# Optimization experiments

Measured on AMD Instinct MI355X. Metric: run time of the kernel, lower is better.

## Reference

```python
import jax, jax.numpy as jnp
import numpy as np

B, T, H, NH, HD = 2, 2048, 2048, 16, 128


def setup_inputs() -> dict:
    key = jax.random.key(0)
    k1, k2, k3 = jax.random.split(key, 3)
    hidden_states = jax.random.normal(k1, (B, T, H), dtype=jnp.float32)
    w_qkv = jax.random.normal(k2, (3 * H, H), dtype=jnp.float32) * (1.0 / np.sqrt(H))
    w_out = jax.random.normal(k3, (H, H), dtype=jnp.float32) * (1.0 / np.sqrt(H))
    return {"hidden_states": hidden_states, "w_qkv": w_qkv, "w_out": w_out}


def reference(hidden_states, w_qkv, w_out):
    scale = 1.0 / np.sqrt(HD)
    # qkv projection: torch Linear is x @ W.T with W [out, in]
    qkv = jnp.einsum('bth,oh->bto', hidden_states, w_qkv)  # [B, T, 3H]
    q, k, v = jnp.split(qkv, 3, axis=2)
    # [B, NH, T, HD]
    q = q.reshape(B, T, NH, HD).transpose(0, 2, 1, 3)
    k = k.reshape(B, T, NH, HD).transpose(0, 2, 1, 3)
    v = v.reshape(B, T, NH, HD).transpose(0, 2, 1, 3)
    scores = jnp.einsum('bhqd,bhkd->bhqk', q, k) * scale  # [B, NH, T, T]
    mask = jnp.tril(jnp.ones((T, T), dtype=bool))  # causal
    scores = jnp.where(mask[None, None], scores, -jnp.inf)
    probs = jax.nn.softmax(scores, axis=-1)
    attn = jnp.einsum('bhqk,bhkd->bhqd', probs, v)  # [B, NH, T, HD]
    attn = attn.transpose(0, 2, 1, 3).reshape(B, T, H)
    out = jnp.einsum('bth,oh->bto', attn, w_out)
    return out
```

## Files before the change

### kernel.cpp

```cpp
#include <hip/hip_runtime.h>
#include <cstdint>
#include <cstddef>

typedef _Float16 f16x8 __attribute__((ext_vector_type(8)));
typedef _Float16 f16x4 __attribute__((ext_vector_type(4)));
typedef float    f32x4 __attribute__((ext_vector_type(4)));
typedef unsigned short ushort_t;

#define LOG2E 1.4426950408889634f

constexpr int BATCH = 2;
constexpr int TSEQ  = 2048;
constexpr int HID   = 2048;
constexpr int NH    = 16;
constexpr int HD    = 128;
constexpr int GK    = 2048;
constexpr int NKT   = GK / 64;

__device__ inline f32x4 mfma16(f16x8 a, f16x8 b, f32x4 c) {
    return __builtin_amdgcn_mfma_f32_16x16x32_f16(a, b, c, 0, 0, 0);
}

__device__ inline void async_copy16(const void* src, void* dst_lds) {
    __builtin_amdgcn_global_load_lds(
        (const __attribute__((address_space(1))) uint32_t*)src,
        (__attribute__((address_space(3))) uint32_t*)dst_lds, 16, 0, 0);
}

__global__ __launch_bounds__(256)
void cast_f32_f16(const float4* __restrict__ in, f16x4* __restrict__ out, int n4) {
    int i = blockIdx.x * 256 + threadIdx.x;
    if (i >= n4) return;
    float4 v = in[i];
    f16x4 o = { (_Float16)v.x, (_Float16)v.y, (_Float16)v.z, (_Float16)v.w };
    out[i] = o;
}

template <int MODE>
__global__ __launch_bounds__(512, 2)
void gemm_bt(const _Float16* __restrict__ A, const _Float16* __restrict__ B,
             float* __restrict__ C, _Float16* __restrict__ Qo,
             _Float16* __restrict__ Ko, _Float16* __restrict__ Vo, int NB) {
    __shared__ __align__(16) _Float16 As[3][256 * 64];
    __shared__ __align__(16) _Float16 Bs[3][128 * 64];

    const int tid  = threadIdx.x;
    const int lane = tid & 63;
    const int w    = tid >> 6;
    const int l15  = lane & 15;
    const int lq   = lane >> 4;
    const int wr   = w >> 1, wc = w & 1;

    const int bid = (int)blockIdx.x;
    const int cpx = (int)gridDim.x >> 3;
    const int swz = (bid & 7) * cpx + (bid >> 3);
    const int bn  = swz % NB, bm = swz / NB;
    const int m0  = bm * 256, n0 = bn * 128;

    const _Float16* Ab = A + (size_t)m0 * GK;
    const _Float16* Bb = B + (size_t)n0 * GK;

    auto stage = [&](int t, int b) {
        const int k0 = t * 64;
        #pragma unroll
        for (int it = 0; it < 4; ++it) {
            const int slot = it * 512 + tid;
            const int row = slot >> 3, c16 = slot & 7;
            const int srcb = c16 ^ (row & 7);
            async_copy16(Ab + (size_t)row * GK + k0 + srcb * 8,
                         (char*)As[b] + slot * 16);
        }
        #pragma unroll
        for (int it = 0; it < 2; ++it) {
            const int slot = it * 512 + tid;
            const int row = slot >> 3, c16 = slot & 7;
            const int srcb = c16 ^ (row & 7);
            async_copy16(Bb + (size_t)row * GK + k0 + srcb * 8,
                         (char*)Bs[b] + slot * 16);
        }
    };

    f32x4 acc[4][4] = {};

    stage(0, 0);
    stage(1, 1);

    for (int t = 0; t < NKT; ++t) {
        if (t + 1 < NKT) asm volatile("s_waitcnt vmcnt(6)" ::: "memory");
        else             asm volatile("s_waitcnt vmcnt(0)" ::: "memory");
        __builtin_amdgcn_s_barrier();
        __builtin_amdgcn_sched_barrier(0);

        const char* At_ = (const char*)As[t % 3];
        const char* Bt_ = (const char*)Bs[t % 3];

        f16x8 af[4][2], bff[4][2];
        #pragma unroll
        for (int i = 0; i < 4; ++i)
            #pragma unroll
            for (int kk = 0; kk < 2; ++kk) {
                const int ra = wr * 64 + i * 16 + l15;
                af[i][kk]  = *(const f16x8*)(At_ + ra * 128 + (((kk * 4 + lq) ^ (ra & 7)) << 4));
                const int rb = wc * 64 + i * 16 + l15;
                bff[i][kk] = *(const f16x8*)(Bt_ + rb * 128 + (((kk * 4 + lq) ^ (rb & 7)) << 4));
            }

        if (t + 2 < NKT) stage(t + 2, (t + 2) % 3);

        __builtin_amdgcn_s_setprio(1);
        #pragma unroll
        for (int kk = 0; kk < 2; ++kk)
            #pragma unroll
            for (int i = 0; i < 4; ++i)
                #pragma unroll
                for (int j = 0; j < 4; ++j)
                    acc[i][j] = mfma16(af[i][kk], bff[j][kk], acc[i][j]);
        __builtin_amdgcn_s_setprio(0);
    }

    if (MODE == 0) {
        #pragma unroll
        for (int j = 0; j < 4; ++j) {
            const int ncol = n0 + wc * 64 + j * 16 + l15;
            const int which = ncol >> 11;
            const int oo = ncol & 2047;
            const int head = oo >> 7;
            const int d = oo & 127;
            _Float16* dst = (which == 0) ? Qo : (which == 1) ? Ko : Vo;
            const float scl = (which == 0) ? 0.08838834764831845f : 1.0f;
            #pragma unroll
            for (int i = 0; i < 4; ++i) {
                #pragma unroll
                for (int r = 0; r < 4; ++r) {
                    const int m = m0 + wr * 64 + i * 16 + lq * 4 + r;
                    const int b = m >> 11, tt = m & 2047;
                    dst[((size_t)(b * NH + head) * TSEQ + tt) * HD + d] =
                        (_Float16)(acc[i][j][r] * scl);
                }
            }
        }
    } else {
        #pragma unroll
        for (int i = 0; i < 4; ++i)
            #pragma unroll
            for (int j = 0; j < 4; ++j)
                #pragma unroll
                for (int r = 0; r < 4; ++r) {
                    const int m = m0 + wr * 64 + i * 16 + lq * 4 + r;
                    const int n = n0 + wc * 64 + j * 16 + l15;
                    C[(size_t)m * HID + n] = acc[i][j][r];
                }
    }
}

__global__ __launch_bounds__(512)
void attn_fwd(const _Float16* __restrict__ Q, const _Float16* __restrict__ K,
              const _Float16* __restrict__ V, _Float16* __restrict__ O) {
    __shared__ __align__(16) char Ks[2][64 * 256];
    __shared__ __align__(16) char Vt[2][128 * 128];
    __shared__ __align__(16) char Ps[8][2048];

    const int tid  = threadIdx.x;
    const int lane = tid & 63;
    const int w    = tid >> 6;
    const int l15  = lane & 15;
    const int lq   = lane >> 4;

    const int bh   = (int)blockIdx.x & 31;
    const int pair = (int)blockIdx.x >> 5;
    const int b = bh >> 4, h = bh & 15;

    const size_t base = (size_t)bh * TSEQ * HD;
    const _Float16* Qp = Q + base;
    const _Float16* Kp = K + base;
    const _Float16* Vp = V + base;

    uint4 vv[2];
    auto loadV = [&](int t) {
        #pragma unroll
        for (int it = 0; it < 2; ++it) {
            const int c8 = it * 8 + w;
            vv[it] = *(const uint4*)(Vp + (size_t)(t * 64 + lane) * HD + c8 * 8);
        }
    };
    auto stageK = [&](int t, int buf) {
        #pragma unroll
        for (int it = 0; it < 2; ++it) {
            const int slot = it * 512 + tid;
            const int row = slot >> 4, c16 = slot & 15;
            const int srcb = c16 ^ (row & 7);
            async_copy16(Kp + (size_t)(t * 64 + row) * HD + srcb * 8, Ks[buf] + slot * 16);
        }
    };
    auto writeV = [&](int buf) {
        #pragma unroll
        for (int it = 0; it < 2; ++it) {
            const int c8 = it * 8 + w;
            const uint32_t wrd[4] = {vv[it].x, vv[it].y, vv[it].z, vv[it].w};
            #pragma unroll
            for (int p2 = 0; p2 < 4; ++p2) {
                const int d0 = c8 * 8 + p2 * 2, d1 = d0 + 1;
                int b0 = d0 * 128 + lane * 2; b0 ^= (d0 & 7) << 4;
                int b1 = d1 * 128 + lane * 2; b1 ^= (d1 & 7) << 4;
                *(ushort_t*)(Vt[buf] + b0) = (ushort_t)(wrd[p2] & 0xffffu);
                *(ushort_t*)(Vt[buf] + b1) = (ushort_t)(wrd[p2] >> 16);
            }
        }
    };

    char* Pb = Ps[w];

    for (int phase = 0; phase < 2; ++phase) {
        const int qt = phase ? pair : (15 - pair);
        const int q0 = qt * 128;
        const int NT = 2 * qt + 2;

        if (phase) __syncthreads();

        const int qrow = q0 + w * 16 + l15;
        f16x8 qf[4];
        #pragma unroll
        for (int ks = 0; ks < 4; ++ks)
            qf[ks] = *(const f16x8*)(Qp + (size_t)qrow * HD + ks * 32 + lq * 8);

        f32x4 o[8] = {};
        float m_run[4], l_run[4];
        #pragma unroll
        for (int r = 0; r < 4; ++r) { m_run[r] = -1e30f; l_run[r] = 0.0f; }

        loadV(0);
        stageK(0, 0);

        int cur = 0;
        for (int t = 0; t < NT; ++t) {
            writeV(cur);
            __syncthreads();
            if (t + 1 < NT) {
                loadV(t + 1);
                stageK(t + 1, cur ^ 1);
            }

            const int kv0 = t * 64;
            f32x4 s[4] = {};
            __builtin_amdgcn_s_setprio(1);
            #pragma unroll
            for (int ks = 0; ks < 4; ++ks) {
                #pragma unroll
                for (int nf = 0; nf < 4; ++nf) {
                    const int r   = nf * 16 + l15;
                    const int blk = (ks * 4 + lq) ^ (r & 7);
                    const f16x8 kf = *(const f16x8*)(Ks[cur] + r * 256 + blk * 16);
                    s[nf] = mfma16(qf[ks], kf, s[nf]);
                }
            }
            __builtin_amdgcn_s_setprio(0);

            if (kv0 + 63 > q0 + w * 16) {
                #pragma unroll
                for (int nf = 0; nf < 4; ++nf) {
                    const int kvp = kv0 + nf * 16 + l15;
                    #pragma unroll
                    for (int r = 0; r < 4; ++r)
                        if (kvp > q0 + w * 16 + lq * 4 + r) s[nf][r] = -1e30f;
                }
            }

            float tmax[4];
            bool need = false;
            #pragma unroll
            for (int r = 0; r < 4; ++r) {
                float v = fmaxf(fmaxf(s[0][r], s[1][r]), fmaxf(s[2][r], s[3][r]));
                v = fmaxf(v, __shfl_xor(v, 1));
                v = fmaxf(v, __shfl_xor(v, 2));
                v = fmaxf(v, __shfl_xor(v, 4));
                v = fmaxf(v, __shfl_xor(v, 8));
                tmax[r] = v;
                need = need || (v > m_run[r] + 5.0f);
            }
            if (__any(need)) {
                float alpha[4];
                #pragma unroll
                for (int r = 0; r < 4; ++r) {
                    const float mn = fmaxf(m_run[r], tmax[r]);
                    alpha[r] = __builtin_exp2f((m_run[r] - mn) * LOG2E);
                    m_run[r] = mn;
                    l_run[r] *= alpha[r];
                }
                #pragma unroll
                for (int df = 0; df < 8; ++df)
                    #pragma unroll
                    for (int r = 0; r < 4; ++r)
                        o[df][r] *= alpha[r];
            }

            float ps[4] = {0.f, 0.f, 0.f, 0.f};
            #pragma unroll
            for (int nf = 0; nf < 4; ++nf) {
                #pragma unroll
                for (int r = 0; r < 4; ++r) {
                    const float p = __builtin_exp2f((s[nf][r] - m_run[r]) * LOG2E);
                    ps[r] += p;
                    const int qp = lq * 4 + r;
                    int byt = qp * 128 + (nf * 16 + l15) * 2;
                    byt ^= (qp & 7) << 4;
                    union { _Float16 hf; ushort_t u; } cv;
                    cv.hf = (_Float16)p;
                    *(ushort_t*)(Pb + byt) = cv.u;
                }
            }
            #pragma unroll
            for (int r = 0; r < 4; ++r) {
                float v = ps[r];
                v += __shfl_xor(v, 1);
                v += __shfl_xor(v, 2);
                v += __shfl_xor(v, 4);
                v += __shfl_xor(v, 8);
                l_run[r] += v;
            }

            __builtin_amdgcn_s_setprio(1);
            #pragma unroll
            for (int ks2 = 0; ks2 < 2; ++ks2) {
                const int pblk = (ks2 * 4 + lq) ^ (l15 & 7);
                const f16x8 pf = *(const f16x8*)(Pb + l15 * 128 + pblk * 16);
                #pragma unroll
                for (int df = 0; df < 8; ++df) {
                    const int vr   = df * 16 + l15;
                    const int vblk = (ks2 * 4 + lq) ^ (vr & 7);
                    const f16x8 vf = *(const f16x8*)(Vt[cur] + vr * 128 + vblk * 16);
                    o[df] = mfma16(pf, vf, o[df]);
                }
            }
            __builtin_amdgcn_s_setprio(0);
            cur ^= 1;
        }

        #pragma unroll
        for (int r = 0; r < 4; ++r) l_run[r] = 1.0f / l_run[r];
        #pragma unroll
        for (int df = 0; df < 8; ++df) {
            #pragma unroll
            for (int r = 0; r < 4; ++r) {
                const int qg = q0 + w * 16 + lq * 4 + r;
                const int dg = df * 16 + l15;
                O[((size_t)(b * TSEQ + qg)) * HID + h * HD + dg] =
                    (_Float16)(o[df][r] * l_run[r]);
            }
        }
    }
}

extern "C" void kernel_launch(void* const* d_in, const int* in_sizes, int n_in,
                              void* d_out, int out_size, void* d_ws, size_t ws_size,
                              hipStream_t stream) {
    (void)in_sizes; (void)n_in; (void)out_size; (void)ws_size;
    const float* hs   = (const float*)d_in[0];
    const float* wqkv = (const float*)d_in[1];
    const float* wout = (const float*)d_in[2];

    char* ws = (char*)d_ws;
    size_t off = 0;
    _Float16* hs_h   = (_Float16*)(ws + off); off += (size_t)BATCH * TSEQ * HID * 2;
    _Float16* wqkv_h = (_Float16*)(ws + off); off += (size_t)3 * HID * HID * 2;
    _Float16* wout_h = (_Float16*)(ws + off); off += (size_t)HID * HID * 2;
    _Float16* Qh     = (_Float16*)(ws + off); off += (size_t)BATCH * NH * TSEQ * HD * 2;
    _Float16* Kh     = (_Float16*)(ws + off); off += (size_t)BATCH * NH * TSEQ * HD * 2;
    _Float16* Vh     = (_Float16*)(ws + off); off += (size_t)BATCH * NH * TSEQ * HD * 2;
    _Float16* At     = (_Float16*)(ws + off); off += (size_t)BATCH * TSEQ * HID * 2;

    const int n4_hs   = BATCH * TSEQ * HID / 4;
    const int n4_wqkv = 3 * HID * HID / 4;
    const int n4_wout = HID * HID / 4;
    cast_f32_f16<<<dim3((n4_hs   + 255) / 256), dim3(256), 0, stream>>>((const float4*)hs,   (f16x4*)hs_h,   n4_hs);
    cast_f32_f16<<<dim3((n4_wqkv + 255) / 256), dim3(256), 0, stream>>>((const float4*)wqkv, (f16x4*)wqkv_h, n4_wqkv);
    cast_f32_f16<<<dim3((n4_wout + 255) / 256), dim3(256), 0, stream>>>((const float4*)wout, (f16x4*)wout_h, n4_wout);

    gemm_bt<0><<<dim3(768), dim3(512), 0, stream>>>(
        hs_h, wqkv_h, nullptr, Qh, Kh, Vh, 48);

    attn_fwd<<<dim3(256), dim3(512), 0, stream>>>(Qh, Kh, Vh, At);

    gemm_bt<1><<<dim3(256), dim3(512), 0, stream>>>(
        At, wout_h, (float*)d_out, nullptr, nullptr, nullptr, 16);
}
```

Measured before the change: 294.1 us.

## Shrink attention blocks to 64 query rows and compute row sums via MFMA

Attention blocks now cover 64 query rows with 4 waves (256 threads) instead of 128 rows with 8 waves, and the grid doubles to 512 blocks with balanced tile pairing across 32 query tiles. The softmax denominator is no longer built from per-tile shuffle reductions; it comes from an extra MFMA of P against a ones vector. The row-max shuffle reduction now runs only when a rescale is triggered. These changes aim to improve load balance and cut reduction overhead, at the cost of each block reusing each K/V tile for fewer query rows, so K/V traffic rises.

```diff
diff --git a/kernel.cpp b/kernel.cpp
--- a/kernel.cpp
+++ b/kernel.cpp
@@ -153,12 +153,12 @@
     }
 }
 
-__global__ __launch_bounds__(512)
+__global__ __launch_bounds__(256)
 void attn_fwd(const _Float16* __restrict__ Q, const _Float16* __restrict__ K,
               const _Float16* __restrict__ V, _Float16* __restrict__ O) {
     __shared__ __align__(16) char Ks[2][64 * 256];
     __shared__ __align__(16) char Vt[2][128 * 128];
-    __shared__ __align__(16) char Ps[8][2048];
+    __shared__ __align__(16) char Ps[4][2048];
 
     const int tid  = threadIdx.x;
     const int lane = tid & 63;
@@ -175,33 +175,38 @@
     const _Float16* Kp = K + base;
     const _Float16* Vp = V + base;
 
-    uint4 vv[2];
+    const f16x8 ones = { (_Float16)1.f, (_Float16)1.f, (_Float16)1.f, (_Float16)1.f,
+                         (_Float16)1.f, (_Float16)1.f, (_Float16)1.f, (_Float16)1.f };
+
+    uint4 vv[4];
     auto loadV = [&](int t) {
-        #pragma unroll
-        for (int it = 0; it < 2; ++it) {
-            const int c8 = it * 8 + w;
-            vv[it] = *(const uint4*)(Vp + (size_t)(t * 64 + lane) * HD + c8 * 8);
+        const int row = tid & 63;
+        #pragma unroll
+        for (int it = 0; it < 4; ++it) {
+            const int c8 = w * 4 + it;
+            vv[it] = *(const uint4*)(Vp + (size_t)(t * 64 + row) * HD + c8 * 8);
         }
     };
     auto stageK = [&](int t, int buf) {
         #pragma unroll
-        for (int it = 0; it < 2; ++it) {
-            const int slot = it * 512 + tid;
+        for (int it = 0; it < 4; ++it) {
+            const int slot = it * 256 + tid;
             const int row = slot >> 4, c16 = slot & 15;
             const int srcb = c16 ^ (row & 7);
             async_copy16(Kp + (size_t)(t * 64 + row) * HD + srcb * 8, Ks[buf] + slot * 16);
         }
     };
     auto writeV = [&](int buf) {
-        #pragma unroll
-        for (int it = 0; it < 2; ++it) {
-            const int c8 = it * 8 + w;
+        const int row = tid & 63;
+        #pragma unroll
+        for (int it = 0; it < 4; ++it) {
+            const int c8 = w * 4 + it;
             const uint32_t wrd[4] = {vv[it].x, vv[it].y, vv[it].z, vv[it].w};
             #pragma unroll
             for (int p2 = 0; p2 < 4; ++p2) {
                 const int d0 = c8 * 8 + p2 * 2, d1 = d0 + 1;
-                int b0 = d0 * 128 + lane * 2; b0 ^= (d0 & 7) << 4;
-                int b1 = d1 * 128 + lane * 2; b1 ^= (d1 & 7) << 4;
+                int b0 = d0 * 128 + row * 2; b0 ^= (d0 & 7) << 4;
+                int b1 = d1 * 128 + row * 2; b1 ^= (d1 & 7) << 4;
                 *(ushort_t*)(Vt[buf] + b0) = (ushort_t)(wrd[p2] & 0xffffu);
                 *(ushort_t*)(Vt[buf] + b1) = (ushort_t)(wrd[p2] >> 16);
             }
@@ -211,9 +216,9 @@
     char* Pb = Ps[w];
 
     for (int phase = 0; phase < 2; ++phase) {
-        const int qt = phase ? pair : (15 - pair);
-        const int q0 = qt * 128;
-        const int NT = 2 * qt + 2;
+        const int qt = phase ? pair : (31 - pair);
+        const int q0 = qt * 64;
+        const int NT = qt + 1;
 
         if (phase) __syncthreads();
 
@@ -224,9 +229,10 @@
             qf[ks] = *(const f16x8*)(Qp + (size_t)qrow * HD + ks * 32 + lq * 8);
 
         f32x4 o[8] = {};
-        float m_run[4], l_run[4];
-        #pragma unroll
-        for (int r = 0; r < 4; ++r) { m_run[r] = -1e30f; l_run[r] = 0.0f; }
+        f32x4 osum = {};
+        float m_run[4];
+        #pragma unroll
+        for (int r = 0; r < 4; ++r) m_run[r] = -1e30f;
 
         loadV(0);
         stageK(0, 0);
@@ -265,41 +271,39 @@
                 }
             }
 
-            float tmax[4];
             bool need = false;
             #pragma unroll
             for (int r = 0; r < 4; ++r) {
-                float v = fmaxf(fmaxf(s[0][r], s[1][r]), fmaxf(s[2][r], s[3][r]));
-                v = fmaxf(v, __shfl_xor(v, 1));
-                v = fmaxf(v, __shfl_xor(v, 2));
-                v = fmaxf(v, __shfl_xor(v, 4));
-                v = fmaxf(v, __shfl_xor(v, 8));
-                tmax[r] = v;
+                const float v = fmaxf(fmaxf(s[0][r], s[1][r]), fmaxf(s[2][r], s[3][r]));
                 need = need || (v > m_run[r] + 5.0f);
             }
             if (__any(need)) {
                 float alpha[4];
                 #pragma unroll
                 for (int r = 0; r < 4; ++r) {
-                    const float mn = fmaxf(m_run[r], tmax[r]);
+                    float v = fmaxf(fmaxf(s[0][r], s[1][r]), fmaxf(s[2][r], s[3][r]));
+                    v = fmaxf(v, __shfl_xor(v, 1));
+                    v = fmaxf(v, __shfl_xor(v, 2));
+                    v = fmaxf(v, __shfl_xor(v, 4));
+                    v = fmaxf(v, __shfl_xor(v, 8));
+                    const float mn = fmaxf(m_run[r], v);
                     alpha[r] = __builtin_exp2f((m_run[r] - mn) * LOG2E);
                     m_run[r] = mn;
-                    l_run[r] *= alpha[r];
                 }
                 #pragma unroll
                 for (int df = 0; df < 8; ++df)
                     #pragma unroll
                     for (int r = 0; r < 4; ++r)
                         o[df][r] *= alpha[r];
-            }
-
-            float ps[4] = {0.f, 0.f, 0.f, 0.f};
+                #pragma unroll
+                for (int r = 0; r < 4; ++r) osum[r] *= alpha[r];
+            }
+
             #pragma unroll
             for (int nf = 0; nf < 4; ++nf) {
                 #pragma unroll
                 for (int r = 0; r < 4; ++r) {
                     const float p = __builtin_exp2f((s[nf][r] - m_run[r]) * LOG2E);
-                    ps[r] += p;
                     const int qp = lq * 4 + r;
                     int byt = qp * 128 + (nf * 16 + l15) * 2;
                     byt ^= (qp & 7) << 4;
@@ -308,15 +312,6 @@
                     *(ushort_t*)(Pb + byt) = cv.u;
                 }
             }
-            #pragma unroll
-            for (int r = 0; r < 4; ++r) {
-                float v = ps[r];
-                v += __shfl_xor(v, 1);
-                v += __shfl_xor(v, 2);
-                v += __shfl_xor(v, 4);
-                v += __shfl_xor(v, 8);
-                l_run[r] += v;
-            }
 
             __builtin_amdgcn_s_setprio(1);
             #pragma unroll
@@ -330,13 +325,15 @@
                     const f16x8 vf = *(const f16x8*)(Vt[cur] + vr * 128 + vblk * 16);
                     o[df] = mfma16(pf, vf, o[df]);
                 }
+                osum = mfma16(pf, ones, osum);
             }
             __builtin_amdgcn_s_setprio(0);
             cur ^= 1;
         }
 
-        #pragma unroll
-        for (int r = 0; r < 4; ++r) l_run[r] = 1.0f / l_run[r];
+        float rl[4];
+        #pragma unroll
+        for (int r = 0; r < 4; ++r) rl[r] = 1.0f / osum[r];
         #pragma unroll
         for (int df = 0; df < 8; ++df) {
             #pragma unroll
@@ -344,7 +341,7 @@
                 const int qg = q0 + w * 16 + lq * 4 + r;
                 const int dg = df * 16 + l15;
                 O[((size_t)(b * TSEQ + qg)) * HID + h * HD + dg] =
-                    (_Float16)(o[df][r] * l_run[r]);
+                    (_Float16)(o[df][r] * rl[r]);
             }
         }
     }
@@ -378,7 +375,7 @@
     gemm_bt<0><<<dim3(768), dim3(512), 0, stream>>>(
         hs_h, wqkv_h, nullptr, Qh, Kh, Vh, 48);
 
-    attn_fwd<<<dim3(256), dim3(512), 0, stream>>>(Qh, Kh, Vh, At);
+    attn_fwd<<<dim3(512), dim3(256), 0, stream>>>(Qh, Kh, Vh, At);
 
     gemm_bt<1><<<dim3(256), dim3(512), 0, stream>>>(
         At, wout_h, (float*)d_out, nullptr, nullptr, nullptr, 16);
```

Result: faster. 274.1 us (-6.8%).
